# Kernel optimization log

Hardware: AMD Instinct MI355X
Metric: run time of the kernel (lower is better)

The kernel has to match this reference:

```python
import jax, jax.numpy as jnp
import numpy as np
import math

BS, SEQ = 2048, 50
REL, ETYPE = 6, 4
ATT, HEADS, HEAD = 64, 4, 16
HID, OUT = 128, 64


def setup_inputs() -> dict:
    key = jax.random.key(0)
    ks = jax.random.split(key, 20)
    d = {}
    d['input_seqs'] = jax.random.normal(ks[0], (BS, SEQ, 3, 3, REL), jnp.float32)
    d['input_edge_types'] = jax.random.uniform(ks[1], (BS, SEQ, 3, 3, ETYPE), jnp.float32)
    d['input_masks'] = jax.random.randint(ks[2], (BS, SEQ, 3, 3), 0, 2, jnp.int32)
    def lin(k, fin, fout):
        k1, k2 = jax.random.split(k)
        bound = 1.0 / math.sqrt(fin)
        W = jax.random.uniform(k1, (fout, fin), jnp.float32, -bound, bound)
        b = jax.random.uniform(k2, (fout,), jnp.float32, -bound, bound)
        return W, b
    d['W_fus'], d['b_fus'] = lin(ks[3], REL + ETYPE + 9, 64)
    d['Wk'], d['bk'] = lin(ks[4], REL, ATT)
    d['Wq'], d['bq'] = lin(ks[5], 64, ATT)
    d['Wv'], d['bv'] = lin(ks[6], 64, ATT)
    bound = 1.0 / math.sqrt(HID)
    d['W_ih'] = jax.random.uniform(ks[7], (4 * HID, ATT), jnp.float32, -bound, bound)
    d['W_hh'] = jax.random.uniform(ks[8], (4 * HID, HID), jnp.float32, -bound, bound)
    d['b_ih'] = jax.random.uniform(ks[9], (4 * HID,), jnp.float32, -bound, bound)
    d['b_hh'] = jax.random.uniform(ks[10], (4 * HID,), jnp.float32, -bound, bound)
    d['W_out'], d['b_out'] = lin(ks[11], HID, OUT)
    return d


def _lstm_last(xs, W_ih, W_hh, b_ih, b_hh):
    # xs: (seq, bs, ATT); torch LSTM gate order i,f,g,o. Returns last hidden state.
    b = b_ih + b_hh
    def step(carry, x):
        h, c = carry
        gates = x @ W_ih.T + h @ W_hh.T + b
        i, f, g, o = jnp.split(gates, 4, axis=-1)
        i, f, o = jax.nn.sigmoid(i), jax.nn.sigmoid(f), jax.nn.sigmoid(o)
        g = jnp.tanh(g)
        c = f * c + i * g
        h = o * jnp.tanh(c)
        return (h, c), None
    h0 = jnp.zeros((xs.shape[1], HID), xs.dtype)
    (h, _), _ = jax.lax.scan(step, (h0, h0), xs)
    return h


def reference(input_seqs, input_edge_types, input_masks, W_fus, b_fus, Wk, bk, Wq, bq, Wv, bv, W_ih, W_hh, b_ih, b_hh, W_out, b_out):
    bs, seq = input_seqs.shape[0], input_seqs.shape[1]
    # location one-hot for the 3x3 neighborhood
    loc = jnp.broadcast_to(jnp.eye(9, dtype=input_seqs.dtype).reshape(3, 3, 9), (bs, seq, 3, 3, 9))
    edge_info = jnp.concatenate([input_seqs, input_edge_types, loc], axis=-1)
    edge_info = edge_info @ W_fus.T + b_fus                 # (bs, seq, 3, 3, 64)
    edge_info = edge_info.reshape(bs, seq, 9, 64)
    self_info = input_seqs[:, :, 1, 1]                       # (bs, seq, REL)
    # key from self state (same for all 9 slots), query/value from edge info
    key = (self_info @ Wk.T + bk).reshape(bs, seq, 1, HEADS, HEAD)     # broadcast over 9
    query = (edge_info @ Wq.T + bq).reshape(bs, seq, 9, HEADS, HEAD)
    value = (edge_info @ Wv.T + bv).reshape(bs, seq, 9, HEADS, HEAD)
    # att: dot over head dim -> (bs, seq, heads, 9)
    att = jnp.einsum('bsnhd,bsnhd->bshn', jnp.broadcast_to(key, query.shape), query) / math.sqrt(HEAD)
    mask9 = input_masks.reshape(bs, seq, 1, 9)               # broadcast over heads
    att = jnp.where(mask9 == 0, jnp.float32(-1e10), att)
    att = jax.nn.softmax(att, axis=-1)                       # (bs, seq, heads, 9)
    ctx = jnp.einsum('bshn,bsnhd->bshd', att, value)         # (bs, seq, heads, head)
    ctx = ctx.reshape(bs, seq, ATT).transpose(1, 0, 2)       # (seq, bs, ATT)
    h_last = _lstm_last(ctx, W_ih, W_hh, b_ih, b_hh)         # (bs, HID)
    return h_last @ W_out.T + b_out                          # (bs, OUT)
```

## Files before the change

kernel.cpp:

```cpp
#include <hip/hip_runtime.h>
#include <math.h>

#define BS   2048
#define SEQ  50
#define NPOS (BS * SEQ)

typedef __attribute__((ext_vector_type(8))) short bf16x8;
typedef __attribute__((ext_vector_type(4))) float f32x4;

__device__ __forceinline__ float sigf(float x) { return 1.0f / (1.0f + __expf(-x)); }
__device__ __forceinline__ float tanhfast(float x) {
    float e = __expf(2.0f * x);
    return 1.0f - 2.0f / (e + 1.0f);
}
__device__ __forceinline__ unsigned short bfrn(float x) {
    unsigned int u = __float_as_uint(x);
    u += 0x7FFFu + ((u >> 16) & 1u);
    return (unsigned short)(u >> 16);
}
__device__ __forceinline__ float bf2f(unsigned short h) {
    return __uint_as_float(((unsigned int)h) << 16);
}

#define FMA4(A, X, W) \
    A = fmaf((X).x, (W).x, A); A = fmaf((X).y, (W).y, A); \
    A = fmaf((X).z, (W).z, A); A = fmaf((X).w, (W).w, A);

__device__ float Wvf_d[640];
__device__ float Ce_d[576];
__device__ float Ag_d[280];
__device__ float Bd_d[252];

__global__ __launch_bounds__(512) void prep_all(
    const float* __restrict__ Wih, const float* __restrict__ Whh,
    bf16x8* __restrict__ whF, bf16x8* __restrict__ wiF,
    const float* __restrict__ Wf, const float* __restrict__ bf,
    const float* __restrict__ Wq, const float* __restrict__ bq,
    const float* __restrict__ Wv,
    const float* __restrict__ Wk, const float* __restrict__ bk)
{
    __shared__ float sG[640];
    __shared__ float sD[576];

    if (blockIdx.x < 48) {
        int id = blockIdx.x * 512 + threadIdx.x;
        const float* src;
        bf16x8* dst;
        int p;
        if (id < 16384) {
            int l = id & 63, frag = id >> 6;
            p = frag & 1;
            int kc = (frag >> 1) & 3, ti = (frag >> 3) & 3, w = frag >> 5;
            int n  = (w + 8 * ti) * 16 + (l & 15);
            int k0 = kc * 32 + (l >> 4) * 8;
            src = &Whh[n * 128 + k0];
            dst = &whF[frag * 64 + l];
        } else {
            int id2 = id - 16384;
            int l = id2 & 63, frag = id2 >> 6;
            p = frag & 1;
            int kc = (frag >> 1) & 1, tile = frag >> 2;
            int n  = tile * 16 + (l & 15);
            int k0 = kc * 32 + (l >> 4) * 8;
            src = &Wih[n * 64 + k0];
            dst = &wiF[frag * 64 + l];
        }
        bf16x8 v;
        #pragma unroll
        for (int j = 0; j < 8; ++j) {
            float x = src[j];
            unsigned short hi = bfrn(x);
            unsigned short r  = p ? bfrn(x - bf2f(hi)) : hi;
            v[j] = (short)r;
        }
        *dst = v;
        return;
    }

    if (blockIdx.x < 51) {
        int i = (blockIdx.x - 48) * 512 + threadIdx.x;
        if (i >= 1216) return;
        if (i < 640) {
            int o = i / 10, k = i % 10;
            float s = 0.f;
            #pragma unroll 8
            for (int j = 0; j < 64; ++j) s = fmaf(Wv[o * 64 + j], Wf[j * 19 + k], s);
            Wvf_d[i] = s;
        } else {
            int i2 = i - 640;
            int o = i2 / 9, e = i2 % 9;
            float s = 0.f;
            #pragma unroll 8
            for (int j = 0; j < 64; ++j)
                s = fmaf(Wf[j * 19 + 10 + e] + bf[j], Wv[o * 64 + j], s);
            Ce_d[i2] = s;
        }
        return;
    }

    const int t = threadIdx.x;
    for (int i = t; i < 1216; i += 512) {
        if (i < 640) {
            int n = i / 10, k = i % 10;
            float s = 0.f;
            #pragma unroll 8
            for (int j = 0; j < 64; ++j) s = fmaf(Wq[n * 64 + j], Wf[j * 19 + k], s);
            sG[i] = s;
        } else {
            int i2 = i - 640;
            int e = i2 >> 6, n = i2 & 63;
            float s = bq[n];
            #pragma unroll 8
            for (int j = 0; j < 64; ++j)
                s = fmaf(Wf[j * 19 + 10 + e] + bf[j], Wq[n * 64 + j], s);
            sD[i2] = s;
        }
    }
    __syncthreads();
    for (int i = t; i < 532; i += 512) {
        if (i < 280) {
            int h = i / 70, rem = i % 70, k = rem / 7, jj = rem % 7;
            float s = 0.f;
            #pragma unroll
            for (int d = 0; d < 16; ++d) {
                int n = h * 16 + d;
                float wkj = (jj < 6) ? Wk[n * 6 + jj] : bk[n];
                s = fmaf(wkj, sG[n * 10 + k], s);
            }
            Ag_d[i] = s;
        } else {
            int i4 = i - 280;
            int e = i4 / 28, rem = i4 % 28, h = rem / 7, jj = rem % 7;
            float s = 0.f;
            #pragma unroll
            for (int d = 0; d < 16; ++d) {
                int n = h * 16 + d;
                float wkj = (jj < 6) ? Wk[n * 6 + jj] : bk[n];
                s = fmaf(wkj, sD[e * 64 + n], s);
            }
            Bd_d[i4] = s;
        }
    }
}

__global__ __launch_bounds__(64, 4) void edge_attn_ctx(
    const float* __restrict__ seqs,
    const float* __restrict__ ets,
    const int*   __restrict__ masks,
    const float* __restrict__ bv,
    float* __restrict__ ctx)
{
    const int o = threadIdx.x;
    const int j = o & 15, h = o >> 4;
    const int j6 = j * 6, j4 = j * 4;

    const int jA = (j < 10) ? j : 9;
    const int jB = (j < 9)  ? j : 8;
    float Agr[7], Bdr[7];
    #pragma unroll
    for (int q = 0; q < 7; ++q) Agr[q] = Ag_d[(h * 10 + jA) * 7 + q];
    #pragma unroll
    for (int q = 0; q < 7; ++q) Bdr[q] = Bd_d[(jB * 4 + h) * 7 + q];
    float Wvfr[10];
    #pragma unroll
    for (int k = 0; k < 10; ++k) Wvfr[k] = Wvf_d[o * 10 + k];
    const float bvr = bv[o];
    float Cer[9];
    #pragma unroll
    for (int e = 0; e < 9; ++e) Cer[e] = Ce_d[o * 9 + e] + bvr;

    const bool selR = (j < 6);
    const int jc = selR ? j : 0;
    const int jm = (j >= 6) ? (j - 6) : 0;

    float r_seq = 0.f, r_et = 0.f; int r_mask = 0;
    if (o < 54) r_seq  = seqs[blockIdx.x * 54 + o];
    if (o < 36) r_et   = ets[blockIdx.x * 36 + o];
    if (o < 9)  r_mask = masks[blockIdx.x * 9 + o];

    for (int p = blockIdx.x; p < NPOS; p += gridDim.x) {
        const float cs = r_seq, cet = r_et; const int cm = r_mask;

        {
            int pn = p + gridDim.x;
            if (pn < NPOS) {
                if (o < 54) r_seq  = seqs[pn * 54 + o];
                if (o < 36) r_et   = ets[pn * 36 + o];
                if (o < 9)  r_mask = masks[pn * 9 + o];
            }
        }

        float c0 = __shfl(cs, 24), c1 = __shfl(cs, 25), c2 = __shfl(cs, 26),
              c3 = __shfl(cs, 27), c4 = __shfl(cs, 28), c5 = __shfl(cs, 29);

        float g = Agr[6];
        g = fmaf(c0, Agr[0], g); g = fmaf(c1, Agr[1], g);
        g = fmaf(c2, Agr[2], g); g = fmaf(c3, Agr[3], g);
        g = fmaf(c4, Agr[4], g); g = fmaf(c5, Agr[5], g);
        float tt = Bdr[6];
        tt = fmaf(c0, Bdr[0], tt); tt = fmaf(c1, Bdr[1], tt);
        tt = fmaf(c2, Bdr[2], tt); tt = fmaf(c3, Bdr[3], tt);
        tt = fmaf(c4, Bdr[4], tt); tt = fmaf(c5, Bdr[5], tt);

        float a = tt;
        #pragma unroll
        for (int k = 0; k < 6; ++k)
            a = fmaf(__shfl(cs, j6 + k), __shfl(g, k, 16), a);
        #pragma unroll
        for (int k = 6; k < 10; ++k)
            a = fmaf(__shfl(cet, j4 + (k - 6)), __shfl(g, k, 16), a);
        a *= 0.25f;
        int mk = __shfl(cm, j);
        a = (mk == 0) ? -1.0e10f : a;
        if (j >= 9) a = -3.0e38f;

        float mx = a;
        mx = fmaxf(mx, __shfl_xor(mx, 1, 16));
        mx = fmaxf(mx, __shfl_xor(mx, 2, 16));
        mx = fmaxf(mx, __shfl_xor(mx, 4, 16));
        mx = fmaxf(mx, __shfl_xor(mx, 8, 16));
        float ex = __expf(a - mx);
        float ss = ex;
        ss += __shfl_xor(ss, 1, 16);
        ss += __shfl_xor(ss, 2, 16);
        ss += __shfl_xor(ss, 4, 16);
        ss += __shfl_xor(ss, 8, 16);

        float exe[9];
        #pragma unroll
        for (int e = 0; e < 9; ++e) exe[e] = __shfl(ex, e, 16);

        float rb = 0.f;
        #pragma unroll
        for (int e = 0; e < 9; ++e) {
            float xa = __shfl(cs,  e * 6 + jc);
            float xb = __shfl(cet, e * 4 + jm);
            rb = fmaf(exe[e], selR ? xa : xb, rb);
        }

        float acc = 0.f;
        #pragma unroll
        for (int k = 0; k < 10; ++k)
            acc = fmaf(__shfl(rb, k, 16), Wvfr[k], acc);
        #pragma unroll
        for (int e = 0; e < 9; ++e)
            acc = fmaf(exe[e], Cer[e], acc);
        ctx[p * 64 + o] = acc * (1.0f / ss);
    }
}

#define MFMA16(A, B, C) __builtin_amdgcn_mfma_f32_16x16x32_bf16(A, B, C, 0, 0, 0)
#define MM4(F, W0, W1, W2, W3) \
    a0 = MFMA16(F, W0, a0); a1 = MFMA16(F, W1, a1); \
    a2 = MFMA16(F, W2, a2); a3 = MFMA16(F, W3, a3);

#define HPASS \
    MM4(hfh[0], whr[0][0][0], whr[1][0][0], whr[2][0][0], whr[3][0][0]) \
    MM4(hfh[1], whr[0][1][0], whr[1][1][0], whr[2][1][0], whr[3][1][0]) \
    MM4(hfh[2], whr[0][2][0], whr[1][2][0], whr[2][2][0], whr[3][2][0]) \
    MM4(hfh[3], whr[0][3][0], whr[1][3][0], whr[2][3][0], whr[3][3][0]) \
    MM4(hfl[0], whr[0][0][0], whr[1][0][0], whr[2][0][0], whr[3][0][0]) \
    MM4(hfl[1], whr[0][1][0], whr[1][1][0], whr[2][1][0], whr[3][1][0]) \
    MM4(hfl[2], whr[0][2][0], whr[1][2][0], whr[2][2][0], whr[3][2][0]) \
    MM4(hfl[3], whr[0][3][0], whr[1][3][0], whr[2][3][0], whr[3][3][0]) \
    MM4(hfh[0], whr[0][0][1], whr[1][0][1], whr[2][0][1], whr[3][0][1]) \
    MM4(hfh[1], whr[0][1][1], whr[1][1][1], whr[2][1][1], whr[3][1][1]) \
    MM4(hfh[2], whr[0][2][1], whr[1][2][1], whr[2][2][1], whr[3][2][1]) \
    MM4(hfh[3], whr[0][3][1], whr[1][3][1], whr[2][3][1], whr[3][3][1])

#define REDIST_E(ch, g0, g1) { \
    float s2_ = __shfl_xor(ch[2], 32), s3_ = __shfl_xor(ch[3], 32); \
    g0 = lolq ? ch[0] : s2_;  g1 = lolq ? ch[1] : s3_; }
#define REDIST_O(ch, g0, g1) { \
    float s0_ = __shfl_xor(ch[0], 32), s1_ = __shfl_xor(ch[1], 32); \
    g0 = lolq ? s0_ : ch[2];  g1 = lolq ? s1_ : ch[3]; }

#define PWBODY(gi0,gf0,gg0,go0,gi1,gf1,gg1,go1, WB0, WB1) { \
    float i0_ = sigf(gi0 + bi), f0_ = sigf(gf0 + bff); \
    float gA_ = tanhfast(gg0 + bg), o0_ = sigf(go0 + bo); \
    c20 = fmaf(f0_, c20, i0_ * gA_); \
    float hv0_ = o0_ * tanhfast(c20); \
    float i1_ = sigf(gi1 + bi), f1_ = sigf(gf1 + bff); \
    float gB_ = tanhfast(gg1 + bg), o1_ = sigf(go1 + bo); \
    c21 = fmaf(f1_, c21, i1_ * gB_); \
    float hv1_ = o1_ * tanhfast(c21); \
    unsigned short hh0_ = bfrn(hv0_), hh1_ = bfrn(hv1_); \
    unsigned short hl0_ = bfrn(hv0_ - bf2f(hh0_)), hl1_ = bfrn(hv1_ - bf2f(hh1_)); \
    *(unsigned short*)((char*)s_hh + (WB0)) = hh0_; \
    *(unsigned short*)((char*)s_hl + (WB0)) = hl0_; \
    *(unsigned short*)((char*)s_hh + (WB1)) = hh1_; \
    *(unsigned short*)((char*)s_hl + (WB1)) = hl1_; }

__global__ __launch_bounds__(512, 2) void lstm_mfma(
    const float*  __restrict__ ctx,
    const bf16x8* __restrict__ whF,
    const bf16x8* __restrict__ wiFg,
    const float*  __restrict__ b_ih, const float* __restrict__ b_hh,
    const float*  __restrict__ W_out, const float* __restrict__ b_out,
    float* __restrict__ out)
{
    const int t  = threadIdx.x;
    const int w  = t >> 6, l = t & 63;
    const int lm = l & 15, lq = l >> 4;
    const int row0 = blockIdx.x * 8;

    __shared__ bf16x8 s_wi[8192];
    __shared__ unsigned short s_xh[1024], s_xl[1024];
    __shared__ unsigned short s_hh[4096], s_hl[4096];

    for (int i = t; i < 8192; i += 512) s_wi[i] = wiFg[i];
    for (int i = t; i < 1024; i += 512) { s_xh[i] = 0; s_xl[i] = 0; }
    for (int i = t; i < 4096; i += 512) { s_hh[i] = 0; s_hl[i] = 0; }

    bf16x8 whr[4][4][2];
    #pragma unroll
    for (int ti = 0; ti < 4; ++ti)
        #pragma unroll
        for (int kc = 0; kc < 4; ++kc)
            #pragma unroll
            for (int p = 0; p < 2; ++p)
                whr[ti][kc][p] = whF[(((w * 4 + ti) * 4 + kc) * 2 + p) * 64 + l];

    const int m = w * 16 + lm;
    const float bi  = b_ih[m]       + b_hh[m];
    const float bff = b_ih[128 + m] + b_hh[128 + m];
    const float bg  = b_ih[256 + m] + b_hh[256 + m];
    const float bo  = b_ih[384 + m] + b_hh[384 + m];

    const int  urb  = ((lq & 1) << 2) | (lq & 2);
    const bool lolq = (lq < 2);
    float c20 = 0.f, c21 = 0.f;

    const int xrow  = t >> 5;
    const int xl32  = t & 31;
    const int srow  = xrow & 7;
    const int spair = xrow >> 3;
    const float2* ctx2 = (const float2*)ctx;
    const int xbase = (row0 + srow) * SEQ + spair;
    const int xwb   = xrow * 128 + ((4 * xl32) ^ ((xrow & 7) << 4));
    const int swzr  = (lm & 7) << 4;
    const int hwb_m = 32 * w + 2 * lm;
    const int wb0e = 4096 + (8 + urb) * 256 + (hwb_m ^ (urb << 4));
    const int wb1e = 4096 + (9 + urb) * 256 + (hwb_m ^ ((urb + 1) << 4));
    const int wb0o = urb * 256 + (hwb_m ^ (urb << 4));
    const int wb1o = (urb + 1) * 256 + (hwb_m ^ ((urb + 1) << 4));

    float2 xv = ctx2[xbase * 32 + xl32];

    for (int u = 0; u < SEQ / 2; ++u) {
        {
            unsigned short xh0 = bfrn(xv.x), xh1 = bfrn(xv.y);
            unsigned short xl0 = bfrn(xv.x - bf2f(xh0)), xl1 = bfrn(xv.y - bf2f(xh1));
            *(unsigned int*)((char*)s_xh + xwb) = (unsigned int)xh0 | ((unsigned int)xh1 << 16);
            *(unsigned int*)((char*)s_xl + xwb) = (unsigned int)xl0 | ((unsigned int)xl1 << 16);
        }
        __syncthreads();

        float2 xvn = make_float2(0.f, 0.f);
        if (u + 1 < SEQ / 2) xvn = ctx2[(xbase + 2 * u + 2) * 32 + xl32];

        bf16x8 hfh[4], hfl[4];
        if (u > 0) {
            #pragma unroll
            for (int kc = 0; kc < 4; ++kc) {
                int b = lm * 256 + ((kc * 64 + lq * 16) ^ swzr);
                hfh[kc] = *(const bf16x8*)((const char*)s_hh + b);
                hfl[kc] = *(const bf16x8*)((const char*)s_hl + b);
            }
        }
        bf16x8 xfh[2], xfl[2];
        #pragma unroll
        for (int kc = 0; kc < 2; ++kc) {
            int b = lm * 128 + ((kc * 64 + lq * 16) ^ swzr);
            xfh[kc] = *(const bf16x8*)((const char*)s_xh + b);
            xfl[kc] = *(const bf16x8*)((const char*)s_xl + b);
        }

        f32x4 a0 = {0.f,0.f,0.f,0.f}, a1 = a0, a2 = a0, a3 = a0;

        if (u > 0) { HPASS }

        #pragma unroll
        for (int kc = 0; kc < 2; ++kc) {
            bf16x8 wihi[4], wilo[4];
            #pragma unroll
            for (int ti = 0; ti < 4; ++ti) {
                int base = (((w + 8 * ti) * 2 + kc) * 2) * 64 + l;
                wihi[ti] = s_wi[base];
                wilo[ti] = s_wi[base + 64];
            }
            MM4(xfh[kc], wihi[0], wihi[1], wihi[2], wihi[3])
            MM4(xfl[kc], wihi[0], wihi[1], wihi[2], wihi[3])
            MM4(xfh[kc], wilo[0], wilo[1], wilo[2], wilo[3])
        }

        {
            float gi0, gi1, gf0, gf1, gg0, gg1, go0, go1;
            REDIST_E(a0, gi0, gi1)
            REDIST_E(a1, gf0, gf1)
            REDIST_E(a2, gg0, gg1)
            REDIST_E(a3, go0, go1)
            PWBODY(gi0, gf0, gg0, go0, gi1, gf1, gg1, go1, wb0e, wb1e)
        }

        __syncthreads();
        #pragma unroll
        for (int kc = 0; kc < 4; ++kc) {
            int b = 4096 + lm * 256 + ((kc * 64 + lq * 16) ^ swzr);
            hfh[kc] = *(const bf16x8*)((const char*)s_hh + b);
            hfl[kc] = *(const bf16x8*)((const char*)s_hl + b);
        }
        HPASS

        {
            float gi0, gi1, gf0, gf1, gg0, gg1, go0, go1;
            REDIST_O(a0, gi0, gi1)
            REDIST_O(a1, gf0, gf1)
            REDIST_O(a2, gg0, gg1)
            REDIST_O(a3, go0, go1)
            PWBODY(gi0, gf0, gg0, go0, gi1, gf1, gg1, go1, wb0o, wb1o)
        }
        xv = xvn;
    }
    __syncthreads();

    {
        const int row = t >> 5;
        if (row < 8) {
            const int j0 = t & 31, j1 = (t & 31) + 32;
            const int rswz = (row & 7) << 4;
            float accA = b_out[j0], accB = b_out[j1];
            #pragma unroll
            for (int kq = 0; kq < 16; ++kq) {
                int b = row * 256 + ((kq * 16) ^ rswz);
                bf16x8 hh8 = *(const bf16x8*)((const char*)s_hh + b);
                bf16x8 hl8 = *(const bf16x8*)((const char*)s_hl + b);
                #pragma unroll
                for (int e = 0; e < 8; ++e) {
                    float h = bf2f((unsigned short)hh8[e]) + bf2f((unsigned short)hl8[e]);
                    int k = kq * 8 + e;
                    accA = fmaf(h, W_out[j0 * 128 + k], accA);
                    accB = fmaf(h, W_out[j1 * 128 + k], accB);
                }
            }
            out[(row0 + row) * 64 + j0] = accA;
            out[(row0 + row) * 64 + j1] = accB;
        }
    }
}

extern "C" void kernel_launch(void* const* d_in, const int* in_sizes, int n_in,
                              void* d_out, int out_size, void* d_ws, size_t ws_size,
                              hipStream_t stream) {
    (void)in_sizes; (void)n_in; (void)out_size; (void)ws_size;
    const float* seqs  = (const float*)d_in[0];
    const float* ets   = (const float*)d_in[1];
    const int*   masks = (const int*)d_in[2];
    const float* Wf  = (const float*)d_in[3];
    const float* bf  = (const float*)d_in[4];
    const float* Wk  = (const float*)d_in[5];
    const float* bk  = (const float*)d_in[6];
    const float* Wq  = (const float*)d_in[7];
    const float* bq  = (const float*)d_in[8];
    const float* Wv  = (const float*)d_in[9];
    const float* bv  = (const float*)d_in[10];
    const float* Wih = (const float*)d_in[11];
    const float* Whh = (const float*)d_in[12];
    const float* bih = (const float*)d_in[13];
    const float* bhh = (const float*)d_in[14];
    const float* Wo  = (const float*)d_in[15];
    const float* bo  = (const float*)d_in[16];

    char* ws = (char*)d_ws;
    bf16x8* whF = (bf16x8*)(ws);
    bf16x8* wiF = (bf16x8*)(ws + 262144);
    float*  ctx = (float*) (ws + 262144 + 131072);

    hipLaunchKernelGGL(prep_all, dim3(52), dim3(512), 0, stream,
                       Wih, Whh, whF, wiF, Wf, bf, Wq, bq, Wv, Wk, bk);
    hipLaunchKernelGGL(edge_attn_ctx, dim3(4096), dim3(64), 0, stream,
                       seqs, ets, masks, bv, ctx);
    hipLaunchKernelGGL(lstm_mfma, dim3(256), dim3(512), 0, stream,
                       ctx, whF, wiF, bih, bhh, Wo, bo, (float*)d_out);
}
```

Measured before the change: 290.8 us.

## Process two positions per block via shared memory instead of wavefront shuffles

Rewrites the edge-attention kernel so each 64-thread block handles two positions per iteration, staging inputs and intermediates (gate vectors, scores, exponentials, reductions) in shared memory rather than moving them with cross-lane shuffles. Thread-to-work mapping is compacted so 40 or 36 lanes do the useful work, and the softmax is computed with serial reads instead of butterfly reductions. The aim is to cut shuffle instruction count and raise instruction-level parallelism, at the cost of several __syncthreads barriers per iteration and idle lanes. The loop stride is now hardcoded to 8192 with an offset of 4096, which assumes a grid of exactly 4096 blocks.

```diff
diff --git a/kernel.cpp b/kernel.cpp
--- a/kernel.cpp
+++ b/kernel.cpp
@@ -150,17 +150,18 @@
     const float* __restrict__ bv,
     float* __restrict__ ctx)
 {
-    const int o = threadIdx.x;
-    const int j = o & 15, h = o >> 4;
-    const int j6 = j * 6, j4 = j * 4;
-
-    const int jA = (j < 10) ? j : 9;
-    const int jB = (j < 9)  ? j : 8;
+    const int o   = threadIdx.x;
+    const int h_o = o >> 4;
+    const int lg  = (o < 40) ? o : 0;
+    const int gh  = lg / 10, gk = lg % 10;
+    const int la  = (o < 36) ? o : 0;
+    const int ah  = la / 9,  ae = la % 9;
+
     float Agr[7], Bdr[7];
     #pragma unroll
-    for (int q = 0; q < 7; ++q) Agr[q] = Ag_d[(h * 10 + jA) * 7 + q];
+    for (int q = 0; q < 7; ++q) Agr[q] = Ag_d[(gh * 10 + gk) * 7 + q];
     #pragma unroll
-    for (int q = 0; q < 7; ++q) Bdr[q] = Bd_d[(jB * 4 + h) * 7 + q];
+    for (int q = 0; q < 7; ++q) Bdr[q] = Bd_d[(ae * 4 + ah) * 7 + q];
     float Wvfr[10];
     #pragma unroll
     for (int k = 0; k < 10; ++k) Wvfr[k] = Wvf_d[o * 10 + k];
@@ -169,83 +170,140 @@
     #pragma unroll
     for (int e = 0; e < 9; ++e) Cer[e] = Ce_d[o * 9 + e] + bvr;
 
-    const bool selR = (j < 6);
-    const int jc = selR ? j : 0;
-    const int jm = (j >= 6) ? (j - 6) : 0;
-
-    float r_seq = 0.f, r_et = 0.f; int r_mask = 0;
-    if (o < 54) r_seq  = seqs[blockIdx.x * 54 + o];
-    if (o < 36) r_et   = ets[blockIdx.x * 36 + o];
-    if (o < 9)  r_mask = masks[blockIdx.x * 9 + o];
-
-    for (int p = blockIdx.x; p < NPOS; p += gridDim.x) {
-        const float cs = r_seq, cet = r_et; const int cm = r_mask;
+    __shared__ float sqA[54], seA[36], sgA[40], saA[36], sxA[36], srA[40];
+    __shared__ float sqB[54], seB[36], sgB[40], saB[36], sxB[36], srB[40];
+    __shared__ int   smA[9], smB[9];
+
+    float rsA = 0.f, reA = 0.f, rsB = 0.f, reB = 0.f;
+    int   rmA = 0, rmB = 0;
+    {
+        int pA = blockIdx.x, pB = pA + 4096;
+        if (o < 54) rsA = seqs[pA * 54 + o];
+        if (o < 36) reA = ets[pA * 36 + o];
+        if (o < 9)  rmA = masks[pA * 9 + o];
+        if (pB < NPOS) {
+            if (o < 54) rsB = seqs[pB * 54 + o];
+            if (o < 36) reB = ets[pB * 36 + o];
+            if (o < 9)  rmB = masks[pB * 9 + o];
+        }
+    }
+
+    for (int p = blockIdx.x; p < NPOS; p += 8192) {
+        const int  pB  = p + 4096;
+        const bool okB = pB < NPOS;
+
+        if (o < 54) { sqA[o] = rsA; sqB[o] = rsB; }
+        if (o < 36) { seA[o] = reA; seB[o] = reB; }
+        if (o < 9)  { smA[o] = rmA; smB[o] = rmB; }
+        __syncthreads();
 
         {
-            int pn = p + gridDim.x;
+            int pn = p + 8192, pnB = pn + 4096;
             if (pn < NPOS) {
-                if (o < 54) r_seq  = seqs[pn * 54 + o];
-                if (o < 36) r_et   = ets[pn * 36 + o];
-                if (o < 9)  r_mask = masks[pn * 9 + o];
-            }
-        }
-
-        float c0 = __shfl(cs, 24), c1 = __shfl(cs, 25), c2 = __shfl(cs, 26),
-              c3 = __shfl(cs, 27), c4 = __shfl(cs, 28), c5 = __shfl(cs, 29);
-
-        float g = Agr[6];
-        g = fmaf(c0, Agr[0], g); g = fmaf(c1, Agr[1], g);
-        g = fmaf(c2, Agr[2], g); g = fmaf(c3, Agr[3], g);
-        g = fmaf(c4, Agr[4], g); g = fmaf(c5, Agr[5], g);
-        float tt = Bdr[6];
-        tt = fmaf(c0, Bdr[0], tt); tt = fmaf(c1, Bdr[1], tt);
-        tt = fmaf(c2, Bdr[2], tt); tt = fmaf(c3, Bdr[3], tt);
-        tt = fmaf(c4, Bdr[4], tt); tt = fmaf(c5, Bdr[5], tt);
-
-        float a = tt;
-        #pragma unroll
-        for (int k = 0; k < 6; ++k)
-            a = fmaf(__shfl(cs, j6 + k), __shfl(g, k, 16), a);
-        #pragma unroll
-        for (int k = 6; k < 10; ++k)
-            a = fmaf(__shfl(cet, j4 + (k - 6)), __shfl(g, k, 16), a);
-        a *= 0.25f;
-        int mk = __shfl(cm, j);
-        a = (mk == 0) ? -1.0e10f : a;
-        if (j >= 9) a = -3.0e38f;
-
-        float mx = a;
-        mx = fmaxf(mx, __shfl_xor(mx, 1, 16));
-        mx = fmaxf(mx, __shfl_xor(mx, 2, 16));
-        mx = fmaxf(mx, __shfl_xor(mx, 4, 16));
-        mx = fmaxf(mx, __shfl_xor(mx, 8, 16));
-        float ex = __expf(a - mx);
-        float ss = ex;
-        ss += __shfl_xor(ss, 1, 16);
-        ss += __shfl_xor(ss, 2, 16);
-        ss += __shfl_xor(ss, 4, 16);
-        ss += __shfl_xor(ss, 8, 16);
-
-        float exe[9];
-        #pragma unroll
-        for (int e = 0; e < 9; ++e) exe[e] = __shfl(ex, e, 16);
-
-        float rb = 0.f;
-        #pragma unroll
-        for (int e = 0; e < 9; ++e) {
-            float xa = __shfl(cs,  e * 6 + jc);
-            float xb = __shfl(cet, e * 4 + jm);
-            rb = fmaf(exe[e], selR ? xa : xb, rb);
-        }
-
-        float acc = 0.f;
-        #pragma unroll
-        for (int k = 0; k < 10; ++k)
-            acc = fmaf(__shfl(rb, k, 16), Wvfr[k], acc);
-        #pragma unroll
-        for (int e = 0; e < 9; ++e)
-            acc = fmaf(exe[e], Cer[e], acc);
-        ctx[p * 64 + o] = acc * (1.0f / ss);
+                if (o < 54) rsA = seqs[pn * 54 + o];
+                if (o < 36) reA = ets[pn * 36 + o];
+                if (o < 9)  rmA = masks[pn * 9 + o];
+            }
+            if (pnB < NPOS) {
+                if (o < 54) rsB = seqs[pnB * 54 + o];
+                if (o < 36) reB = ets[pnB * 36 + o];
+                if (o < 9)  rmB = masks[pnB * 9 + o];
+            }
+        }
+
+        float ttA = 0.f, ttB = 0.f;
+        {
+            float a0 = sqA[24], a1 = sqA[25], a2 = sqA[26],
+                  a3 = sqA[27], a4 = sqA[28], a5 = sqA[29];
+            float b0 = sqB[24], b1 = sqB[25], b2 = sqB[26],
+                  b3 = sqB[27], b4 = sqB[28], b5 = sqB[29];
+            if (o < 40) {
+                float gA = Agr[6], gB = Agr[6];
+                gA = fmaf(a0, Agr[0], gA); gB = fmaf(b0, Agr[0], gB);
+                gA = fmaf(a1, Agr[1], gA); gB = fmaf(b1, Agr[1], gB);
+                gA = fmaf(a2, Agr[2], gA); gB = fmaf(b2, Agr[2], gB);
+                gA = fmaf(a3, Agr[3], gA); gB = fmaf(b3, Agr[3], gB);
+                gA = fmaf(a4, Agr[4], gA); gB = fmaf(b4, Agr[4], gB);
+                gA = fmaf(a5, Agr[5], gA); gB = fmaf(b5, Agr[5], gB);
+                sgA[o] = gA; sgB[o] = gB;
+            }
+            if (o < 36) {
+                ttA = Bdr[6]; ttB = Bdr[6];
+                ttA = fmaf(a0, Bdr[0], ttA); ttB = fmaf(b0, Bdr[0], ttB);
+                ttA = fmaf(a1, Bdr[1], ttA); ttB = fmaf(b1, Bdr[1], ttB);
+                ttA = fmaf(a2, Bdr[2], ttA); ttB = fmaf(b2, Bdr[2], ttB);
+                ttA = fmaf(a3, Bdr[3], ttA); ttB = fmaf(b3, Bdr[3], ttB);
+                ttA = fmaf(a4, Bdr[4], ttA); ttB = fmaf(b4, Bdr[4], ttB);
+                ttA = fmaf(a5, Bdr[5], ttA); ttB = fmaf(b5, Bdr[5], ttB);
+            }
+        }
+        __syncthreads();
+
+        float aA = 0.f, aB = 0.f;
+        if (o < 36) {
+            aA = ttA; aB = ttB;
+            #pragma unroll
+            for (int k = 0; k < 6; ++k) {
+                aA = fmaf(sqA[ae * 6 + k], sgA[ah * 10 + k], aA);
+                aB = fmaf(sqB[ae * 6 + k], sgB[ah * 10 + k], aB);
+            }
+            #pragma unroll
+            for (int k = 0; k < 4; ++k) {
+                aA = fmaf(seA[ae * 4 + k], sgA[ah * 10 + 6 + k], aA);
+                aB = fmaf(seB[ae * 4 + k], sgB[ah * 10 + 6 + k], aB);
+            }
+            aA *= 0.25f; aB *= 0.25f;
+            if (smA[ae] == 0) aA = -1.0e10f;
+            if (smB[ae] == 0) aB = -1.0e10f;
+            saA[o] = aA; saB[o] = aB;
+        }
+        __syncthreads();
+
+        float exA = 0.f, exB = 0.f;
+        if (o < 36) {
+            float mxA = saA[ah * 9 + 0], mxB = saB[ah * 9 + 0];
+            #pragma unroll
+            for (int e = 1; e < 9; ++e) {
+                mxA = fmaxf(mxA, saA[ah * 9 + e]);
+                mxB = fmaxf(mxB, saB[ah * 9 + e]);
+            }
+            exA = __expf(aA - mxA); exB = __expf(aB - mxB);
+            sxA[o] = exA; sxB[o] = exB;
+        }
+        __syncthreads();
+
+        if (o < 40) {
+            float rbA = 0.f, rbB = 0.f;
+            #pragma unroll
+            for (int e = 0; e < 9; ++e) {
+                float xA = (gk < 6) ? sqA[e * 6 + gk] : seA[e * 4 + (gk - 6)];
+                float xB = (gk < 6) ? sqB[e * 6 + gk] : seB[e * 4 + (gk - 6)];
+                rbA = fmaf(sxA[gh * 9 + e], xA, rbA);
+                rbB = fmaf(sxB[gh * 9 + e], xB, rbB);
+            }
+            srA[o] = rbA; srB[o] = rbB;
+        }
+        __syncthreads();
+
+        {
+            float ssA = 0.f, ssB = 0.f;
+            #pragma unroll
+            for (int e = 0; e < 9; ++e) { ssA += sxA[h_o * 9 + e]; ssB += sxB[h_o * 9 + e]; }
+            float acA = 0.f, acB = 0.f;
+            #pragma unroll
+            for (int k = 0; k < 10; ++k) {
+                acA = fmaf(srA[h_o * 10 + k], Wvfr[k], acA);
+                acB = fmaf(srB[h_o * 10 + k], Wvfr[k], acB);
+            }
+            #pragma unroll
+            for (int e = 0; e < 9; ++e) {
+                acA = fmaf(sxA[h_o * 9 + e], Cer[e], acA);
+                acB = fmaf(sxB[h_o * 9 + e], Cer[e], acB);
+            }
+            ctx[p * 64 + o] = acA * (1.0f / ssA);
+            if (okB) ctx[pB * 64 + o] = acB * (1.0f / ssB);
+        }
+        __syncthreads();
     }
 }
 
```

Measured after the change: 248.5 us. 1.17x faster.

## Map one position per thread in edge attention and register-cache LSTM input weights

Applied to the files above, without the earlier changes.

The edge attention kernel changes from one 64-thread wavefront per position, which relied heavily on cross-lane shuffles, to one thread per position. Each thread computes all heads, the softmax and the 64 context outputs serially, reading the constant tables through uniform loads. The cost is uncoalesced strided loads of inputs and stores of ctx, plus high register pressure. Separately, the LSTM kernel keeps its input-projection weights in registers instead of shared memory, which removes per-step LDS reads and the initial 128KB staging. The bias is now added after normalization instead of being folded into the per-slot constants, which is mathematically equivalent.

```diff
diff --git a/kernel.cpp b/kernel.cpp
--- a/kernel.cpp
+++ b/kernel.cpp
@@ -143,109 +143,109 @@
     }
 }
 
-__global__ __launch_bounds__(64, 4) void edge_attn_ctx(
+__global__ __launch_bounds__(256) void edge_attn_ctx(
     const float* __restrict__ seqs,
     const float* __restrict__ ets,
     const int*   __restrict__ masks,
     const float* __restrict__ bv,
     float* __restrict__ ctx)
 {
-    const int o = threadIdx.x;
-    const int j = o & 15, h = o >> 4;
-    const int j6 = j * 6, j4 = j * 4;
-
-    const int jA = (j < 10) ? j : 9;
-    const int jB = (j < 9)  ? j : 8;
-    float Agr[7], Bdr[7];
-    #pragma unroll
-    for (int q = 0; q < 7; ++q) Agr[q] = Ag_d[(h * 10 + jA) * 7 + q];
-    #pragma unroll
-    for (int q = 0; q < 7; ++q) Bdr[q] = Bd_d[(jB * 4 + h) * 7 + q];
-    float Wvfr[10];
-    #pragma unroll
-    for (int k = 0; k < 10; ++k) Wvfr[k] = Wvf_d[o * 10 + k];
-    const float bvr = bv[o];
-    float Cer[9];
-    #pragma unroll
-    for (int e = 0; e < 9; ++e) Cer[e] = Ce_d[o * 9 + e] + bvr;
-
-    const bool selR = (j < 6);
-    const int jc = selR ? j : 0;
-    const int jm = (j >= 6) ? (j - 6) : 0;
-
-    float r_seq = 0.f, r_et = 0.f; int r_mask = 0;
-    if (o < 54) r_seq  = seqs[blockIdx.x * 54 + o];
-    if (o < 36) r_et   = ets[blockIdx.x * 36 + o];
-    if (o < 9)  r_mask = masks[blockIdx.x * 9 + o];
-
-    for (int p = blockIdx.x; p < NPOS; p += gridDim.x) {
-        const float cs = r_seq, cet = r_et; const int cm = r_mask;
-
-        {
-            int pn = p + gridDim.x;
-            if (pn < NPOS) {
-                if (o < 54) r_seq  = seqs[pn * 54 + o];
-                if (o < 36) r_et   = ets[pn * 36 + o];
-                if (o < 9)  r_mask = masks[pn * 9 + o];
-            }
-        }
-
-        float c0 = __shfl(cs, 24), c1 = __shfl(cs, 25), c2 = __shfl(cs, 26),
-              c3 = __shfl(cs, 27), c4 = __shfl(cs, 28), c5 = __shfl(cs, 29);
-
-        float g = Agr[6];
-        g = fmaf(c0, Agr[0], g); g = fmaf(c1, Agr[1], g);
-        g = fmaf(c2, Agr[2], g); g = fmaf(c3, Agr[3], g);
-        g = fmaf(c4, Agr[4], g); g = fmaf(c5, Agr[5], g);
-        float tt = Bdr[6];
-        tt = fmaf(c0, Bdr[0], tt); tt = fmaf(c1, Bdr[1], tt);
-        tt = fmaf(c2, Bdr[2], tt); tt = fmaf(c3, Bdr[3], tt);
-        tt = fmaf(c4, Bdr[4], tt); tt = fmaf(c5, Bdr[5], tt);
-
-        float a = tt;
-        #pragma unroll
-        for (int k = 0; k < 6; ++k)
-            a = fmaf(__shfl(cs, j6 + k), __shfl(g, k, 16), a);
-        #pragma unroll
-        for (int k = 6; k < 10; ++k)
-            a = fmaf(__shfl(cet, j4 + (k - 6)), __shfl(g, k, 16), a);
-        a *= 0.25f;
-        int mk = __shfl(cm, j);
-        a = (mk == 0) ? -1.0e10f : a;
-        if (j >= 9) a = -3.0e38f;
-
-        float mx = a;
-        mx = fmaxf(mx, __shfl_xor(mx, 1, 16));
-        mx = fmaxf(mx, __shfl_xor(mx, 2, 16));
-        mx = fmaxf(mx, __shfl_xor(mx, 4, 16));
-        mx = fmaxf(mx, __shfl_xor(mx, 8, 16));
-        float ex = __expf(a - mx);
-        float ss = ex;
-        ss += __shfl_xor(ss, 1, 16);
-        ss += __shfl_xor(ss, 2, 16);
-        ss += __shfl_xor(ss, 4, 16);
-        ss += __shfl_xor(ss, 8, 16);
-
-        float exe[9];
-        #pragma unroll
-        for (int e = 0; e < 9; ++e) exe[e] = __shfl(ex, e, 16);
-
-        float rb = 0.f;
-        #pragma unroll
-        for (int e = 0; e < 9; ++e) {
-            float xa = __shfl(cs,  e * 6 + jc);
-            float xb = __shfl(cet, e * 4 + jm);
-            rb = fmaf(exe[e], selR ? xa : xb, rb);
-        }
-
+    const int p = blockIdx.x * 256 + threadIdx.x;
+    if (p >= NPOS) return;
+    const float* sp = seqs + p * 54;
+    const float* ep = ets  + p * 36;
+    const int*   mp = masks + p * 9;
+
+    const float s0 = sp[24], s1 = sp[25], s2 = sp[26],
+                s3 = sp[27], s4 = sp[28], s5 = sp[29];
+
+    float g[4][10];
+    #pragma unroll
+    for (int h = 0; h < 4; ++h)
+        #pragma unroll
+        for (int k = 0; k < 10; ++k) {
+            const float* a = &Ag_d[(h * 10 + k) * 7];
+            float v = a[6];
+            v = fmaf(s0, a[0], v); v = fmaf(s1, a[1], v);
+            v = fmaf(s2, a[2], v); v = fmaf(s3, a[3], v);
+            v = fmaf(s4, a[4], v); v = fmaf(s5, a[5], v);
+            g[h][k] = v;
+        }
+
+    float att[9][4];
+    float mx0 = -3.0e38f, mx1 = -3.0e38f, mx2 = -3.0e38f, mx3 = -3.0e38f;
+    #pragma unroll
+    for (int e = 0; e < 9; ++e) {
+        float r0 = sp[e*6+0], r1 = sp[e*6+1], r2 = sp[e*6+2],
+              r3 = sp[e*6+3], r4 = sp[e*6+4], r5 = sp[e*6+5];
+        float r6 = ep[e*4+0], r7 = ep[e*4+1], r8 = ep[e*4+2], r9 = ep[e*4+3];
+        const int mk = mp[e];
+        #pragma unroll
+        for (int h = 0; h < 4; ++h) {
+            const float* b = &Bd_d[(e * 4 + h) * 7];
+            float a = b[6];
+            a = fmaf(s0, b[0], a); a = fmaf(s1, b[1], a);
+            a = fmaf(s2, b[2], a); a = fmaf(s3, b[3], a);
+            a = fmaf(s4, b[4], a); a = fmaf(s5, b[5], a);
+            a = fmaf(r0, g[h][0], a); a = fmaf(r1, g[h][1], a);
+            a = fmaf(r2, g[h][2], a); a = fmaf(r3, g[h][3], a);
+            a = fmaf(r4, g[h][4], a); a = fmaf(r5, g[h][5], a);
+            a = fmaf(r6, g[h][6], a); a = fmaf(r7, g[h][7], a);
+            a = fmaf(r8, g[h][8], a); a = fmaf(r9, g[h][9], a);
+            a *= 0.25f;
+            a = (mk == 0) ? -1.0e10f : a;
+            att[e][h] = a;
+            if (h == 0) mx0 = fmaxf(mx0, a);
+            if (h == 1) mx1 = fmaxf(mx1, a);
+            if (h == 2) mx2 = fmaxf(mx2, a);
+            if (h == 3) mx3 = fmaxf(mx3, a);
+        }
+    }
+
+    float ss0 = 0.f, ss1 = 0.f, ss2 = 0.f, ss3 = 0.f;
+    #pragma unroll
+    for (int e = 0; e < 9; ++e) {
+        att[e][0] = __expf(att[e][0] - mx0); ss0 += att[e][0];
+        att[e][1] = __expf(att[e][1] - mx1); ss1 += att[e][1];
+        att[e][2] = __expf(att[e][2] - mx2); ss2 += att[e][2];
+        att[e][3] = __expf(att[e][3] - mx3); ss3 += att[e][3];
+    }
+
+    float rb[4][10];
+    #pragma unroll
+    for (int h = 0; h < 4; ++h)
+        #pragma unroll
+        for (int k = 0; k < 10; ++k) rb[h][k] = 0.f;
+    #pragma unroll
+    for (int e = 0; e < 9; ++e) {
+        float r0 = sp[e*6+0], r1 = sp[e*6+1], r2 = sp[e*6+2],
+              r3 = sp[e*6+3], r4 = sp[e*6+4], r5 = sp[e*6+5];
+        float r6 = ep[e*4+0], r7 = ep[e*4+1], r8 = ep[e*4+2], r9 = ep[e*4+3];
+        #pragma unroll
+        for (int h = 0; h < 4; ++h) {
+            const float w = att[e][h];
+            rb[h][0] = fmaf(w, r0, rb[h][0]); rb[h][1] = fmaf(w, r1, rb[h][1]);
+            rb[h][2] = fmaf(w, r2, rb[h][2]); rb[h][3] = fmaf(w, r3, rb[h][3]);
+            rb[h][4] = fmaf(w, r4, rb[h][4]); rb[h][5] = fmaf(w, r5, rb[h][5]);
+            rb[h][6] = fmaf(w, r6, rb[h][6]); rb[h][7] = fmaf(w, r7, rb[h][7]);
+            rb[h][8] = fmaf(w, r8, rb[h][8]); rb[h][9] = fmaf(w, r9, rb[h][9]);
+        }
+    }
+    const float iv0 = 1.f / ss0, iv1 = 1.f / ss1, iv2 = 1.f / ss2, iv3 = 1.f / ss3;
+
+    float* cp = ctx + p * 64;
+    #pragma unroll
+    for (int o = 0; o < 64; ++o) {
+        const int h = o >> 4;
+        const float inv = (h == 0) ? iv0 : (h == 1) ? iv1 : (h == 2) ? iv2 : iv3;
+        const float* wv = &Wvf_d[o * 10];
+        const float* ce = &Ce_d[o * 9];
         float acc = 0.f;
         #pragma unroll
-        for (int k = 0; k < 10; ++k)
-            acc = fmaf(__shfl(rb, k, 16), Wvfr[k], acc);
-        #pragma unroll
-        for (int e = 0; e < 9; ++e)
-            acc = fmaf(exe[e], Cer[e], acc);
-        ctx[p * 64 + o] = acc * (1.0f / ss);
+        for (int k = 0; k < 10; ++k) acc = fmaf(rb[h][k], wv[k], acc);
+        #pragma unroll
+        for (int e = 0; e < 9; ++e) acc = fmaf(att[e][h], ce[e], acc);
+        cp[o] = acc * inv + bv[o];
     }
 }
 
@@ -304,11 +304,9 @@
     const int lm = l & 15, lq = l >> 4;
     const int row0 = blockIdx.x * 8;
 
-    __shared__ bf16x8 s_wi[8192];
     __shared__ unsigned short s_xh[1024], s_xl[1024];
     __shared__ unsigned short s_hh[4096], s_hl[4096];
 
-    for (int i = t; i < 8192; i += 512) s_wi[i] = wiFg[i];
     for (int i = t; i < 1024; i += 512) { s_xh[i] = 0; s_xl[i] = 0; }
     for (int i = t; i < 4096; i += 512) { s_hh[i] = 0; s_hl[i] = 0; }
 
@@ -320,6 +318,15 @@
             #pragma unroll
             for (int p = 0; p < 2; ++p)
                 whr[ti][kc][p] = whF[(((w * 4 + ti) * 4 + kc) * 2 + p) * 64 + l];
+
+    bf16x8 wir[2][4][2];
+    #pragma unroll
+    for (int kc = 0; kc < 2; ++kc)
+        #pragma unroll
+        for (int ti = 0; ti < 4; ++ti)
+            #pragma unroll
+            for (int p = 0; p < 2; ++p)
+                wir[kc][ti][p] = wiFg[(((w + 8 * ti) * 2 + kc) * 2 + p) * 64 + l];
 
     const int m = w * 16 + lm;
     const float bi  = b_ih[m]       + b_hh[m];
@@ -382,16 +389,9 @@
 
         #pragma unroll
         for (int kc = 0; kc < 2; ++kc) {
-            bf16x8 wihi[4], wilo[4];
-            #pragma unroll
-            for (int ti = 0; ti < 4; ++ti) {
-                int base = (((w + 8 * ti) * 2 + kc) * 2) * 64 + l;
-                wihi[ti] = s_wi[base];
-                wilo[ti] = s_wi[base + 64];
-            }
-            MM4(xfh[kc], wihi[0], wihi[1], wihi[2], wihi[3])
-            MM4(xfl[kc], wihi[0], wihi[1], wihi[2], wihi[3])
-            MM4(xfh[kc], wilo[0], wilo[1], wilo[2], wilo[3])
+            MM4(xfh[kc], wir[kc][0][0], wir[kc][1][0], wir[kc][2][0], wir[kc][3][0])
+            MM4(xfl[kc], wir[kc][0][0], wir[kc][1][0], wir[kc][2][0], wir[kc][3][0])
+            MM4(xfh[kc], wir[kc][0][1], wir[kc][1][1], wir[kc][2][1], wir[kc][3][1])
         }
 
         {
@@ -478,7 +478,7 @@
 
     hipLaunchKernelGGL(prep_all, dim3(52), dim3(512), 0, stream,
                        Wih, Whh, whF, wiF, Wf, bf, Wq, bq, Wv, Wk, bk);
-    hipLaunchKernelGGL(edge_attn_ctx, dim3(4096), dim3(64), 0, stream,
+    hipLaunchKernelGGL(edge_attn_ctx, dim3(400), dim3(256), 0, stream,
                        seqs, ets, masks, bv, ctx);
     hipLaunchKernelGGL(lstm_mfma, dim3(256), dim3(512), 0, stream,
                        ctx, whF, wiF, bih, bhh, Wo, bo, (float*)d_out);
```

After: 246.0 us. -15.4%, faster.
